# Kernel tuning notes

Hardware: AMD Instinct MI355X
Metric: run time of the kernel (lower is better)

## Reference

```python
import jax, jax.numpy as jnp
import numpy as np

B, T, D = 1, 2048, 2048
HQ, HKV = 32, 8
DH = D // HQ          # 64
NREP = HQ // HKV      # 4


def _apply_rope(x, cos, sin):
    # x: (B, T, H, DH); cos/sin: (T, DH//2). Complex multiply on interleaved pairs:
    # (x0 + i*x1) * (c + i*s) -> (x0*c - x1*s, x0*s + x1*c)
    b, t, h, d = x.shape
    xr = x.reshape(b, t, h, d // 2, 2)
    x0, x1 = xr[..., 0], xr[..., 1]
    c = cos[:t][None, :, None, :]
    s = sin[:t][None, :, None, :]
    o0 = x0 * c - x1 * s
    o1 = x0 * s + x1 * c
    return jnp.stack([o0, o1], axis=-1).reshape(b, t, h, d)


def setup_inputs() -> dict:
    key = jax.random.key(0)
    ks = jax.random.split(key, 6)
    w = 0.02
    x = jax.random.normal(ks[0], (B, T, D), dtype=jnp.float32)
    Wq = jax.random.normal(ks[1], (HQ * DH, D), dtype=jnp.float32) * w
    Wk = jax.random.normal(ks[2], (HKV * DH, D), dtype=jnp.float32) * w
    Wv = jax.random.normal(ks[3], (HKV * DH, D), dtype=jnp.float32) * w
    Wo = jax.random.normal(ks[4], (D, HQ * DH), dtype=jnp.float32) * w
    # standard RoPE frequencies, theta = 10000
    inv_freq = 1.0 / (10000.0 ** (np.arange(0, DH, 2, dtype=np.float32) / DH))
    angles = np.arange(T, dtype=np.float32)[:, None] * inv_freq[None, :]  # (T, DH//2)
    rope_cos = jnp.asarray(np.cos(angles))
    rope_sin = jnp.asarray(np.sin(angles))
    mask = jnp.tril(jnp.ones((T, T), dtype=bool))  # causal
    return {"x": x, "Wq": Wq, "Wk": Wk, "Wv": Wv, "Wo": Wo,
            "rope_cos": rope_cos, "rope_sin": rope_sin, "mask": mask}


def reference(x, Wq, Wk, Wv, Wo, rope_cos, rope_sin, mask):
    b, t, d = x.shape
    q = (x @ Wq.T).reshape(b, t, HQ, DH)
    k = (x @ Wk.T).reshape(b, t, HKV, DH)
    v = (x @ Wv.T).reshape(b, t, HKV, DH)
    q = _apply_rope(q, rope_cos, rope_sin)
    k = _apply_rope(k, rope_cos, rope_sin)
    # GQA: head index = kv_head * NREP + rep (matches torch expand+reshape order)
    qg = q.reshape(b, t, HKV, NREP, DH)
    scale = jnp.sqrt(jnp.float32(DH))
    # scores: (B, HKV, NREP, T, S) without materializing expanded K
    scores = jnp.einsum('bthrd,bshd->bhrts', qg, k) / scale
    scores = jnp.where(mask[None, None, None, :t, :t], scores, -jnp.inf)
    attn = jax.nn.softmax(scores, axis=-1)
    out = jnp.einsum('bhrts,bshd->bthrd', attn, v)  # (B, T, HKV, NREP, DH)
    out = out.reshape(b, t, HQ * DH)
    return out @ Wo.T
```

## Files before the change

kernel.cpp:

```cpp
#include <hip/hip_runtime.h>
#include <math.h>
#include <stdint.h>

static constexpr int T   = 2048;
static constexpr int D   = 2048;
static constexpr int HQ  = 32;
static constexpr int HKV = 8;
static constexpr int DH  = 64;
static constexpr int DKV = HKV * DH;
static constexpr int NQKV = D + 2 * DKV;

typedef float f32x4 __attribute__((ext_vector_type(4)));
typedef __bf16 bf16x8 __attribute__((ext_vector_type(8)));
typedef __bf16 bf16x2 __attribute__((ext_vector_type(2)));
typedef unsigned short u16x8 __attribute__((ext_vector_type(8)));
typedef unsigned short u16x4 __attribute__((ext_vector_type(4)));

__device__ __forceinline__ unsigned short f2bf(float f) {
  union { float f; unsigned u; } v; v.f = f;
  unsigned u = v.u;
  return (unsigned short)((u + 0x7FFFu + ((u >> 16) & 1u)) >> 16);
}
__device__ __forceinline__ float bf2f(unsigned short b) {
  union { unsigned u; float f; } v; v.u = ((unsigned)b) << 16;
  return v.f;
}
__device__ __forceinline__ unsigned pk2bf(float a, float b) {
#if __has_builtin(__builtin_amdgcn_cvt_pk_bf16_f32)
  bf16x2 r = __builtin_amdgcn_cvt_pk_bf16_f32(a, b);
  return __builtin_bit_cast(unsigned, r);
#else
  return (unsigned)f2bf(a) | ((unsigned)f2bf(b) << 16);
#endif
}
__device__ __forceinline__ float fexp2(float x) {
#if __has_builtin(__builtin_amdgcn_exp2f)
  return __builtin_amdgcn_exp2f(x);
#else
  return exp2f(x);
#endif
}
__device__ __forceinline__ float frcp(float x) {
#if __has_builtin(__builtin_amdgcn_rcpf)
  return __builtin_amdgcn_rcpf(x);
#else
  return 1.0f / x;
#endif
}
__device__ __forceinline__ f32x4 mfma16(u16x8 a, u16x8 b, f32x4 c) {
  return __builtin_amdgcn_mfma_f32_16x16x32_bf16(
      __builtin_bit_cast(bf16x8, a), __builtin_bit_cast(bf16x8, b), c, 0, 0, 0);
}
__device__ __forceinline__ void gld16(const unsigned short* g, unsigned short* l) {
  __builtin_amdgcn_global_load_lds(
      (const __attribute__((address_space(1))) unsigned*)g,
      (__attribute__((address_space(3))) unsigned*)l, 16, 0, 0);
}

__global__ __launch_bounds__(256) void cvt_all(const float* __restrict__ x,
                                               const float* __restrict__ Wq,
                                               const float* __restrict__ Wk,
                                               const float* __restrict__ Wv,
                                               const float* __restrict__ Wo,
                                               unsigned short* __restrict__ xb,
                                               unsigned short* __restrict__ wqkv,
                                               unsigned short* __restrict__ wob) {
  int b = blockIdx.x;
  const float* src;
  unsigned short* dst;
  if (b < 2048)      { src = x;  dst = xb; }
  else if (b < 4096) { src = Wq; dst = wqkv;                          b -= 2048; }
  else if (b < 4608) { src = Wk; dst = wqkv + (size_t)D * D;          b -= 4096; }
  else if (b < 5120) { src = Wv; dst = wqkv + (size_t)(D + DKV) * D;  b -= 4608; }
  else               { src = Wo; dst = wob;                           b -= 5120; }
  size_t i = ((size_t)b * 256 + threadIdx.x) * 8;
  float4 a = *(const float4*)(src + i);
  float4 c = *(const float4*)(src + i + 4);
  uint4 r = {pk2bf(a.x, a.y), pk2bf(a.z, a.w), pk2bf(c.x, c.y), pk2bf(c.z, c.w)};
  *(uint4*)(dst + i) = r;
}

template <int EPI>
__global__ __launch_bounds__(256) void gemm_bt_bf16(const unsigned short* __restrict__ A,
                                                    const unsigned short* __restrict__ Bt,
                                                    void* __restrict__ Cv,
                                                    int N, int K,
                                                    const float* __restrict__ cosb,
                                                    const float* __restrict__ sinb) {
  __shared__ alignas(16) unsigned short As[64 * 128];
  __shared__ alignas(16) unsigned short Bs[128 * 128];

  const int bn = blockIdx.x * 128, bm = blockIdx.y * 64;
  const int tid = threadIdx.x, w = tid >> 6, lane = tid & 63;
  const int c = lane & 15, quad = lane >> 4;

  const int r4 = lane >> 4, ch = lane & 15;
  const unsigned short* aRow = A + (size_t)(bm + w * 16 + r4) * K;
  const unsigned short* bRow = Bt + (size_t)(bn + w * 32 + r4) * K;
  unsigned short* AsW = As + (w * 16) * 128;
  unsigned short* BsW = Bs + (w * 32) * 128;

  f32x4 acc[4][2] = {};

  for (int k0 = 0; k0 < K; k0 += 128) {
#pragma unroll
    for (int j = 0; j < 4; j++) {
      const int sch = ch ^ ((j * 4 + r4) & 15);
      gld16(aRow + (size_t)(j * 4) * K + k0 + sch * 8, AsW + j * 4 * 128);
    }
#pragma unroll
    for (int j = 0; j < 8; j++) {
      const int sch = ch ^ ((j * 4 + r4) & 15);
      gld16(bRow + (size_t)(j * 4) * K + k0 + sch * 8, BsW + j * 4 * 128);
    }
    __syncthreads();

#pragma unroll
    for (int ks = 0; ks < 4; ks++) {
      const int slot = (ks * 4 + quad) ^ c;
      u16x8 a[4], b[2];
#pragma unroll
      for (int mi = 0; mi < 4; mi++)
        a[mi] = *(const u16x8*)&As[(mi * 16 + c) * 128 + slot * 8];
#pragma unroll
      for (int ni = 0; ni < 2; ni++)
        b[ni] = *(const u16x8*)&Bs[(w * 32 + ni * 16 + c) * 128 + slot * 8];
#pragma unroll
      for (int mi = 0; mi < 4; mi++)
#pragma unroll
        for (int ni = 0; ni < 2; ni++)
          acc[mi][ni] = mfma16(a[mi], b[ni], acc[mi][ni]);
    }
    __syncthreads();
  }

  if (EPI == 0) {
#pragma unroll
    for (int mi = 0; mi < 4; mi++)
#pragma unroll
      for (int ni = 0; ni < 2; ni++)
#pragma unroll
        for (int r = 0; r < 4; r++) {
          size_t row = (size_t)(bm + mi * 16 + quad * 4 + r);
          size_t col = (size_t)(bn + w * 32 + ni * 16 + c);
          ((float*)Cv)[row * N + col] = acc[mi][ni][r];
        }
  } else if (bn < 2560) {
    const float sc = (bn < 2048) ? 0.125f * 1.44269504088896340736f : 1.0f;
    const float sgn = (c & 1) ? 1.0f : -1.0f;
#pragma unroll
    for (int mi = 0; mi < 4; mi++)
#pragma unroll
      for (int ni = 0; ni < 2; ni++) {
        const int i = ((w * 32 + ni * 16 + c) & 63) >> 1;
#pragma unroll
        for (int r = 0; r < 4; r++) {
          const int t = bm + mi * 16 + quad * 4 + r;
          const float cs = cosb[t * 32 + i];
          const float sn = sinb[t * 32 + i];
          const float val = acc[mi][ni][r];
          const float px = __shfl_xor(val, 1, 64);
          const float outv = (val * cs + sgn * px * sn) * sc;
          ((unsigned short*)Cv)[(size_t)t * N + bn + w * 32 + ni * 16 + c] = f2bf(outv);
        }
      }
  } else {
#pragma unroll
    for (int mi = 0; mi < 4; mi++)
#pragma unroll
      for (int ni = 0; ni < 2; ni++)
#pragma unroll
        for (int r = 0; r < 4; r++) {
          size_t row = (size_t)(bm + mi * 16 + quad * 4 + r);
          size_t col = (size_t)(bn + w * 32 + ni * 16 + c);
          ((unsigned short*)Cv)[row * N + col] = f2bf(acc[mi][ni][r]);
        }
  }
}

__global__ __launch_bounds__(256) void vt_only(const unsigned short* __restrict__ QKV,
                                               unsigned short* __restrict__ VT) {
  __shared__ unsigned short Ts[64][65];
  const int bid = blockIdx.x;
  const int tb = bid & 31, db = bid >> 5;
  const int tid = threadIdx.x;
  const int r = tid >> 2, c0 = (tid & 3) * 16;
  const unsigned short* src = QKV + (size_t)(tb * 64 + r) * NQKV + (D + DKV) + db * 64 + c0;
  *(u16x8*)&Ts[r][c0]     = *(const u16x8*)src;
  *(u16x8*)&Ts[r][c0 + 8] = *(const u16x8*)(src + 8);
  __syncthreads();
  u16x8 a, b;
#pragma unroll
  for (int j = 0; j < 8; j++) a[j] = Ts[c0 + j][r];
#pragma unroll
  for (int j = 0; j < 8; j++) b[j] = Ts[c0 + 8 + j][r];
  unsigned short* dst = VT + (size_t)(db * 64 + r) * T + tb * 64 + c0;
  *(u16x8*)dst = a;
  *(u16x8*)(dst + 8) = b;
}

__global__ __launch_bounds__(256) void attn_kernel(const unsigned short* __restrict__ QKV,
                                                   const unsigned short* __restrict__ VT,
                                                   unsigned short* __restrict__ Ob) {
  const int kh = blockIdx.x;
  const int qt = (int)(gridDim.y - 1 - blockIdx.y);
  const int qbase = qt * 16;
  const int tid = threadIdx.x, w = tid >> 6, lane = tid & 63;
  const int c = lane & 15, quad = lane >> 4;
  const int h = kh * 4 + w;

  __shared__ alignas(16) unsigned short Kt[2][64 * 64];
  __shared__ alignas(16) unsigned short Vt[2][64 * 64];
  __shared__ alignas(16) unsigned short Pb[4 * 16 * 72];

  unsigned short* PbW = Pb + w * 16 * 72;

  u16x8 qf[2];
  {
    const unsigned short* qp = QKV + (size_t)(qbase + c) * NQKV + h * DH + quad * 8;
    qf[0] = *(const u16x8*)qp;
    qf[1] = *(const u16x8*)(qp + 32);
  }

  const int srow = lane >> 3;
  const int sch  = (lane & 7) ^ srow;
  const unsigned short* kgBase = QKV + D + (size_t)(w * 16 + srow) * NQKV + kh * DH + sch * 8;
  const unsigned short* vgBase = VT + (size_t)(kh * DH + w * 16 + srow) * T + sch * 8;

  f32x4 o[4] = {};
  float l = 0.f;

  const int nFull = qt >> 2;

#pragma unroll
  for (int j = 0; j < 2; j++) {
    gld16(kgBase + (size_t)(j * 8) * NQKV, &Kt[0][(w * 16 + j * 8) * 64]);
    gld16(vgBase + (size_t)(j * 8) * T, &Vt[0][(w * 16 + j * 8) * 64]);
  }

  for (int st = 0; st <= nFull; st++) {
    const int cur = st & 1;
    __syncthreads();
    if (st < nFull) {
#pragma unroll
      for (int j = 0; j < 2; j++) {
        gld16(kgBase + ((size_t)(st + 1) * 64 + (size_t)j * 8) * NQKV,
              &Kt[cur ^ 1][(w * 16 + j * 8) * 64]);
        gld16(vgBase + (size_t)(j * 8) * T + (st + 1) * 64,
              &Vt[cur ^ 1][(w * 16 + j * 8) * 64]);
      }
    }

    f32x4 sacc[4] = {};
#pragma unroll
    for (int ks = 0; ks < 2; ks++) {
#pragma unroll
      for (int ni = 0; ni < 4; ni++) {
        const int slot = (ks * 4 + quad) ^ (c & 7);
        u16x8 kf = *(const u16x8*)&Kt[cur][(ni * 16 + c) * 64 + slot * 8];
        sacc[ni] = mfma16(kf, qf[ks], sacc[ni]);
      }
    }

    if (st == nFull) {
      const int qrow = qbase + c;
#pragma unroll
      for (int ni = 0; ni < 4; ni++)
#pragma unroll
        for (int r = 0; r < 4; r++) {
          int key = st * 64 + ni * 16 + quad * 4 + r;
          if (key > qrow) sacc[ni][r] = -INFINITY;
        }
    }

#pragma unroll
    for (int ni = 0; ni < 4; ni++) {
      float p0 = fexp2(sacc[ni][0]);
      float p1 = fexp2(sacc[ni][1]);
      float p2 = fexp2(sacc[ni][2]);
      float p3 = fexp2(sacc[ni][3]);
      l += (p0 + p1) + (p2 + p3);
      uint2 pr = {pk2bf(p0, p1), pk2bf(p2, p3)};
      *(uint2*)&PbW[c * 72 + ni * 16 + quad * 4] = pr;
    }

#pragma unroll
    for (int ks = 0; ks < 2; ks++) {
      u16x8 pf = *(const u16x8*)&PbW[c * 72 + ks * 32 + quad * 8];
#pragma unroll
      for (int ni = 0; ni < 4; ni++) {
        const int slot = (ks * 4 + quad) ^ (c & 7);
        u16x8 vf = *(const u16x8*)&Vt[cur][(ni * 16 + c) * 64 + slot * 8];
        o[ni] = mfma16(pf, vf, o[ni]);
      }
    }
  }

  l += __shfl_xor(l, 16, 64);
  l += __shfl_xor(l, 32, 64);

  float lR[4];
#pragma unroll
  for (int r = 0; r < 4; r++) lR[r] = frcp(__shfl(l, quad * 4 + r, 64));
#pragma unroll
  for (int ni = 0; ni < 4; ni++)
#pragma unroll
    for (int r = 0; r < 4; r++) {
      size_t row = (size_t)(qbase + quad * 4 + r);
      size_t col = (size_t)(h * DH + ni * 16 + c);
      Ob[row * D + col] = f2bf(o[ni][r] * lR[r]);
    }
}

extern "C" void kernel_launch(void* const* d_in, const int* in_sizes, int n_in,
                              void* d_out, int out_size, void* d_ws, size_t ws_size,
                              hipStream_t stream) {
  const float* x  = (const float*)d_in[0];
  const float* Wq = (const float*)d_in[1];
  const float* Wk = (const float*)d_in[2];
  const float* Wv = (const float*)d_in[3];
  const float* Wo = (const float*)d_in[4];
  const float* rc = (const float*)d_in[5];
  const float* rs = (const float*)d_in[6];
  float* out = (float*)d_out;

  char* ws = (char*)d_ws;
  unsigned short* xb   = (unsigned short*)(ws);
  unsigned short* wqkv = (unsigned short*)(ws + (size_t)(8u  << 20));
  unsigned short* wob  = (unsigned short*)(ws + (size_t)(20u << 20));
  unsigned short* qkvb = (unsigned short*)(ws + (size_t)(28u << 20));
  unsigned short* Ab   = xb;
  unsigned short* VT   = wqkv;

  cvt_all<<<dim3(7168), 256, 0, stream>>>(x, Wq, Wk, Wv, Wo, xb, wqkv, wob);

  gemm_bt_bf16<1><<<dim3(NQKV / 128, T / 64), 256, 0, stream>>>(xb, wqkv, qkvb,
                                                                NQKV, D, rc, rs);

  vt_only<<<dim3(256), 256, 0, stream>>>(qkvb, VT);

  attn_kernel<<<dim3(HKV, T / 16), 256, 0, stream>>>(qkvb, VT, Ab);

  gemm_bt_bf16<0><<<dim3(D / 128, T / 64), 256, 0, stream>>>(Ab, wob, out, D, D,
                                                             nullptr, nullptr);
}
```

Baseline: 213.9 us.

## Process two 16-row query tiles per attention block with 8 waves sharing K/V

The attention kernel now launches 512-thread blocks covering 32 query rows: 8 waves, each head's 4 waves replicated for two 16-row sub-tiles, all sharing one double-buffered K/V tile in LDS. This halves K/V global loads per query row and cuts the number of blocks. The block schedule interleaves long and short causal tiles (descending for the first half, ascending for the second) to balance load. The trade-off is larger LDS use for the P buffer, fewer blocks in flight, and extra masked work on the diagonal tile for the lower sub-tile.

```diff
diff --git a/kernel.cpp b/kernel.cpp
--- a/kernel.cpp
+++ b/kernel.cpp
@@ -199,56 +199,52 @@
   *(u16x8*)(dst + 8) = b;
 }
 
-__global__ __launch_bounds__(256) void attn_kernel(const unsigned short* __restrict__ QKV,
-                                                   const unsigned short* __restrict__ VT,
-                                                   unsigned short* __restrict__ Ob) {
+__global__ __launch_bounds__(512, 4) void attn_kernel(const unsigned short* __restrict__ QKV,
+                                                      const unsigned short* __restrict__ VT,
+                                                      unsigned short* __restrict__ Ob) {
   const int kh = blockIdx.x;
-  const int qt = (int)(gridDim.y - 1 - blockIdx.y);
-  const int qbase = qt * 16;
+  const int ny = (int)gridDim.y;
+  const int y = (int)blockIdx.y;
+  const int qt2 = (y < (ny >> 1)) ? (ny - 1 - 2 * y) : (2 * (y - (ny >> 1)));
+  const int qbase = qt2 * 32;
   const int tid = threadIdx.x, w = tid >> 6, lane = tid & 63;
   const int c = lane & 15, quad = lane >> 4;
-  const int h = kh * 4 + w;
+  const int h = kh * 4 + (w & 3);
+  const int sub = w >> 2;
+  const int qbaseW = qbase + sub * 16;
 
   __shared__ alignas(16) unsigned short Kt[2][64 * 64];
   __shared__ alignas(16) unsigned short Vt[2][64 * 64];
-  __shared__ alignas(16) unsigned short Pb[4 * 16 * 72];
+  __shared__ alignas(16) unsigned short Pb[8 * 16 * 72];
 
   unsigned short* PbW = Pb + w * 16 * 72;
 
   u16x8 qf[2];
   {
-    const unsigned short* qp = QKV + (size_t)(qbase + c) * NQKV + h * DH + quad * 8;
+    const unsigned short* qp = QKV + (size_t)(qbaseW + c) * NQKV + h * DH + quad * 8;
     qf[0] = *(const u16x8*)qp;
     qf[1] = *(const u16x8*)(qp + 32);
   }
 
   const int srow = lane >> 3;
   const int sch  = (lane & 7) ^ srow;
-  const unsigned short* kgBase = QKV + D + (size_t)(w * 16 + srow) * NQKV + kh * DH + sch * 8;
-  const unsigned short* vgBase = VT + (size_t)(kh * DH + w * 16 + srow) * T + sch * 8;
+  const unsigned short* kgBase = QKV + D + (size_t)(w * 8 + srow) * NQKV + kh * DH + sch * 8;
+  const unsigned short* vgBase = VT + (size_t)(kh * DH + w * 8 + srow) * T + sch * 8;
 
   f32x4 o[4] = {};
   float l = 0.f;
 
-  const int nFull = qt >> 2;
-
-#pragma unroll
-  for (int j = 0; j < 2; j++) {
-    gld16(kgBase + (size_t)(j * 8) * NQKV, &Kt[0][(w * 16 + j * 8) * 64]);
-    gld16(vgBase + (size_t)(j * 8) * T, &Vt[0][(w * 16 + j * 8) * 64]);
-  }
+  const int nFull = qt2 >> 1;
+
+  gld16(kgBase, &Kt[0][(w * 8) * 64]);
+  gld16(vgBase, &Vt[0][(w * 8) * 64]);
 
   for (int st = 0; st <= nFull; st++) {
     const int cur = st & 1;
     __syncthreads();
     if (st < nFull) {
-#pragma unroll
-      for (int j = 0; j < 2; j++) {
-        gld16(kgBase + ((size_t)(st + 1) * 64 + (size_t)j * 8) * NQKV,
-              &Kt[cur ^ 1][(w * 16 + j * 8) * 64]);
-        gld16(vgBase + (size_t)(j * 8) * T + (st + 1) * 64,
-              &Vt[cur ^ 1][(w * 16 + j * 8) * 64]);
-      }
+      gld16(kgBase + (size_t)(st + 1) * 64 * NQKV, &Kt[cur ^ 1][(w * 8) * 64]);
+      gld16(vgBase + (size_t)(st + 1) * 64,        &Vt[cur ^ 1][(w * 8) * 64]);
     }
 
     f32x4 sacc[4] = {};
@@ -263,7 +259,7 @@
     }
 
     if (st == nFull) {
-      const int qrow = qbase + c;
+      const int qrow = qbaseW + c;
 #pragma unroll
       for (int ni = 0; ni < 4; ni++)
 #pragma unroll
@@ -306,7 +302,7 @@
   for (int ni = 0; ni < 4; ni++)
 #pragma unroll
     for (int r = 0; r < 4; r++) {
-      size_t row = (size_t)(qbase + quad * 4 + r);
+      size_t row = (size_t)(qbaseW + quad * 4 + r);
       size_t col = (size_t)(h * DH + ni * 16 + c);
       Ob[row * D + col] = f2bf(o[ni][r] * lR[r]);
     }
@@ -339,7 +335,7 @@
 
   vt_only<<<dim3(256), 256, 0, stream>>>(qkvb, VT);
 
-  attn_kernel<<<dim3(HKV, T / 16), 256, 0, stream>>>(qkvb, VT, Ab);
+  attn_kernel<<<dim3(HKV, T / 32), 512, 0, stream>>>(qkvb, VT, Ab);
 
   gemm_bt_bf16<0><<<dim3(D / 128, T / 64), 256, 0, stream>>>(Ab, wob, out, D, D,
                                                              nullptr, nullptr);
```

Measured after the change: 218.1 us. About the same (+2.0%).
